# Optimization experiments

Measured on AMD Instinct MI355X. Metric: run time of the kernel, lower is better.

Reference implementation:

```python
import jax, jax.numpy as jnp
import numpy as np

# libmolgrid GridMaker defaults (gnina): resolution 0.5 A, dimension 23.5 A
RES = 0.5
DIM = 23.5
G = int(round(DIM / RES)) + 1  # 48 grid points per axis
N_ATOMS = 800
N_TYPES = 28  # gnina default atom typing


def setup_inputs() -> dict:
    key = jax.random.key(0)
    k1, k2, k3 = jax.random.split(key, 3)
    # atoms spread around the grid center (grid spans +-11.75 A)
    coords = jax.random.normal(k1, (N_ATOMS, 3), dtype=jnp.float32) * 4.0
    # continuous (soft) type vectors in [0,1)
    types = jax.random.uniform(k2, (N_ATOMS, N_TYPES), dtype=jnp.float32)
    # van-der-Waals-like radii in [1.0, 1.8) A
    radii = 1.0 + 0.8 * jax.random.uniform(k3, (N_ATOMS,), dtype=jnp.float32)
    center = jnp.zeros((3,), dtype=jnp.float32)
    return {"center": center, "coords": coords, "types": types, "radii": radii}


def _density(coords, radii, center):
    """Per-atom libmolgrid density on the [G,G,G] grid -> [N,G,G,G].

    f(d) = exp(-2 d^2/r^2)                         for d <  r
         = e^-2 (4 (d/r)^2 - 12 (d/r) + 9)          for r <= d < 1.5 r
         = 0                                        otherwise
    (C1-continuous quadratic tail, libmolgrid defaults grm=1.0, final=1.5).
    """
    origin = center - DIM / 2.0  # [3]
    ax = jnp.arange(G, dtype=jnp.float32) * RES  # [G]
    dx = (origin[0] + ax)[None, :] - coords[:, 0:1]  # [N,G]
    dy = (origin[1] + ax)[None, :] - coords[:, 1:2]
    dz = (origin[2] + ax)[None, :] - coords[:, 2:3]
    d2 = (dx[:, :, None, None] ** 2
          + dy[:, None, :, None] ** 2
          + dz[:, None, None, :] ** 2)  # [N,G,G,G]
    r = radii[:, None, None, None]
    dr2 = d2 / (r * r)
    dr = jnp.sqrt(jnp.maximum(dr2, 1e-12))
    gauss = jnp.exp(-2.0 * dr2)
    inv_e2 = jnp.float32(np.exp(-2.0))
    quad = inv_e2 * (4.0 * dr2 - 12.0 * dr + 9.0)
    return jnp.where(dr < 1.0, gauss, jnp.where(dr < 1.5, quad, 0.0))


def reference(center, coords, types, radii):
    dens = _density(coords, radii, center)  # [N,G,G,G]
    # weight each atom's footprint by its type vector and scatter-sum over atoms
    return jnp.einsum('nxyz,nt->txyz', dens, types)  # [T,G,G,G]
```

## Files before the change

kernel.cpp:

```cpp
#include <hip/hip_runtime.h>

#define GR    48
#define GR2   (GR * GR)
#define GR3   (GR * GR * GR)
#define NA    800
#define NT    28
#define RESF  0.5f
#define HALF_DIM 11.75f
#define INV_E2 0.13533528323661270f

#define TXC   2
#define TYC   2
#define TZC   16
#define NTX   (GR / TXC)
#define NTY   (GR / TYC)
#define NTZ   (GR / TZC)
#define NBLK  (NTX * NTY * NTZ)
#define KB    64
#define KPAD  80

typedef __attribute__((ext_vector_type(8))) short short8;
typedef __attribute__((ext_vector_type(4))) float floatx4;

__device__ inline unsigned short f2bf(float x) {
    unsigned u = __builtin_bit_cast(unsigned, x);
    u = (u + 0x7FFFu + ((u >> 16) & 1u)) >> 16;
    return (unsigned short)u;
}

__global__ __launch_bounds__(256) void c2g_kernel(
    const float* __restrict__ center,
    const float* __restrict__ coords,
    const float* __restrict__ types,
    const float* __restrict__ radii,
    float* __restrict__ out)
{
    __shared__ float4 s_atom[NA];
    __shared__ int    s_ai[NA];
    __shared__ int    s_cnt;
    __shared__ unsigned short s_val[64 * KPAD];
    __shared__ unsigned short s_tT[32 * KPAD];
    __shared__ float  s_out[64 * 33];

    const int tid  = threadIdx.x;
    const int lane = tid & 63;
    const int w    = tid >> 6;
    const int b    = blockIdx.x;
    const int tz   = b % NTZ;
    const int ty   = (b / NTZ) % NTY;
    const int tx   = b / (NTZ * NTY);

    const float ox = center[0] - HALF_DIM;
    const float oy = center[1] - HALF_DIM;
    const float oz = center[2] - HALF_DIM;

    const float bxlo = ox + tx * (TXC * RESF), bxhi = bxlo + (TXC - 1) * RESF;
    const float bylo = oy + ty * (TYC * RESF), byhi = bylo + (TYC - 1) * RESF;
    const float bzlo = oz + tz * (TZC * RESF), bzhi = bzlo + (TZC - 1) * RESF;

    if (tid == 0) s_cnt = 0;
    __syncthreads();

    for (int a0 = 0; a0 < NA; a0 += 256) {
        int a = a0 + tid;
        bool accept = false;
        float ax = 0.f, ay = 0.f, az = 0.f, r = 1.f;
        if (a < NA) {
            ax = coords[3 * a + 0];
            ay = coords[3 * a + 1];
            az = coords[3 * a + 2];
            r  = radii[a];
            float cut = 1.5f * r;
            float ddx = ax - fminf(fmaxf(ax, bxlo), bxhi);
            float ddy = ay - fminf(fmaxf(ay, bylo), byhi);
            float ddz = az - fminf(fmaxf(az, bzlo), bzhi);
            float d2 = fmaf(ddx, ddx, fmaf(ddy, ddy, ddz * ddz));
            accept = d2 < cut * cut;
        }
        unsigned long long m = __ballot(accept);
        if (m) {
            int base = 0;
            if (lane == 0) base = atomicAdd(&s_cnt, __popcll(m));
            base = __shfl(base, 0);
            if (accept) {
                int p = base + __popcll(m & ((1ull << lane) - 1ull));
                s_atom[p] = make_float4(ax, ay, az, 1.0f / (r * r));
                s_ai[p] = a;
            }
        }
    }
    __syncthreads();
    const int cnt = s_cnt;

    const int lzz = lane & 15;
    const int ly2 = (lane >> 4) & 1;
    const int lx2 = lane >> 5;
    const float gx = bxlo + lx2 * RESF;
    const float gy = bylo + ly2 * RESF;
    const float gz = bzlo + lzz * RESF;

    const int lm = lane & 15;
    const int lg = lane >> 4;

    floatx4 acc0 = {0.f, 0.f, 0.f, 0.f};
    floatx4 acc1 = {0.f, 0.f, 0.f, 0.f};

    const int r0 = tid >> 3,         q0 = tid & 7;
    const int r1 = (tid + 256) >> 3, q1 = tid & 7;

    for (int k0 = 0; k0 < cnt; k0 += KB) {
        const int kmax = (cnt - k0 < KB) ? (cnt - k0) : KB;

        float4 tv0 = make_float4(0.f, 0.f, 0.f, 0.f);
        float4 tv1 = tv0;
        if (q0 < 7 && r0 < kmax)
            tv0 = *(const float4*)(types + s_ai[k0 + r0] * NT + q0 * 4);
        if (q1 < 7 && r1 < kmax)
            tv1 = *(const float4*)(types + s_ai[k0 + r1] * NT + q1 * 4);

        unsigned pk[8];
        #pragma unroll
        for (int jj = 0; jj < 8; ++jj) {
            float v[2];
            #pragma unroll
            for (int h = 0; h < 2; ++h) {
                int row = w * 16 + 2 * jj + h;
                float vv = 0.0f;
                if (row < kmax) {
                    float4 at = s_atom[k0 + row];
                    float dx = gx - at.x;
                    float dy = gy - at.y;
                    float dz = gz - at.z;
                    float d2 = fmaf(dx, dx, fmaf(dy, dy, dz * dz));
                    float dr2 = d2 * at.w;
                    float g  = __expf(-2.0f * dr2);
                    float dr = sqrtf(dr2);
                    float q  = INV_E2 * fmaf(4.0f, dr2, fmaf(-12.0f, dr, 9.0f));
                    vv = (dr2 < 1.0f) ? g : ((dr2 < 2.25f) ? q : 0.0f);
                }
                v[h] = vv;
            }
            pk[jj] = (unsigned)f2bf(v[0]) | ((unsigned)f2bf(v[1]) << 16);
        }
        *(uint4*)&s_val[lane * KPAD + w * 16]     = *(uint4*)&pk[0];
        *(uint4*)&s_val[lane * KPAD + w * 16 + 8] = *(uint4*)&pk[4];

        {
            const float* e0 = &tv0.x;
            const float* e1 = &tv1.x;
            #pragma unroll
            for (int i = 0; i < 4; ++i) {
                s_tT[(q0 * 4 + i) * KPAD + r0] = f2bf(e0[i]);
                s_tT[(q1 * 4 + i) * KPAD + r1] = f2bf(e1[i]);
            }
        }
        __syncthreads();

        #pragma unroll
        for (int ks = 0; ks < 2; ++ks) {
            int ko = ks * 32 + lg * 8;
            short8 afr = *(const short8*)&s_val[(w * 16 + lm) * KPAD + ko];
            short8 b0  = *(const short8*)&s_tT[lm * KPAD + ko];
            short8 b1  = *(const short8*)&s_tT[(16 + lm) * KPAD + ko];
            acc0 = __builtin_amdgcn_mfma_f32_16x16x32_bf16(afr, b0, acc0, 0, 0, 0);
            acc1 = __builtin_amdgcn_mfma_f32_16x16x32_bf16(afr, b1, acc1, 0, 0, 0);
        }
        __syncthreads();
    }

    #pragma unroll
    for (int r = 0; r < 4; ++r) {
        int cellO = w * 16 + lg * 4 + r;
        s_out[cellO * 33 + lm]      = acc0[r];
        s_out[cellO * 33 + 16 + lm] = acc1[r];
    }
    __syncthreads();

    #pragma unroll
    for (int i = 0; i < 7; ++i) {
        int idx = i * 256 + tid;
        int t = idx >> 6;
        int c = idx & 63;
        int z = c & 15, y = (c >> 4) & 1, x = c >> 5;
        int gidx = (tx * TXC + x) * GR2 + (ty * TYC + y) * GR + tz * TZC + z;
        out[t * GR3 + gidx] = s_out[c * 33 + t];
    }
}

extern "C" void kernel_launch(void* const* d_in, const int* in_sizes, int n_in,
                              void* d_out, int out_size, void* d_ws, size_t ws_size,
                              hipStream_t stream) {
    const float* center = (const float*)d_in[0];
    const float* coords = (const float*)d_in[1];
    const float* types  = (const float*)d_in[2];
    const float* radii  = (const float*)d_in[3];
    float* out = (float*)d_out;

    c2g_kernel<<<dim3(NBLK), dim3(256), 0, stream>>>(center, coords, types, radii, out);
}
```

Before: 72.06 us.

## Compute density fragments directly in registers and double-buffer type tiles

Swaps the MFMA operand roles so each lane computes its density values straight into the B-fragment registers, which removes the s_val shared-memory staging and one barrier per chunk. Type rows are prefetched from global memory one chunk ahead into a double-buffered LDS tile. The atom list is padded to a multiple of 64 with far-away dummy atoms so the per-row bounds checks go away. Shared memory is also aliased to shrink the footprint, at the cost of extra padding work and a reworked output transpose.

New measurement: 74.72 us. +3.7%, slower.

```diff
diff --git a/kernel.cpp b/kernel.cpp
--- a/kernel.cpp
+++ b/kernel.cpp
@@ -4,6 +4,7 @@
 #define GR2   (GR * GR)
 #define GR3   (GR * GR * GR)
 #define NA    800
+#define NAP   864
 #define NT    28
 #define RESF  0.5f
 #define HALF_DIM 11.75f
@@ -18,6 +19,7 @@
 #define NBLK  (NTX * NTY * NTZ)
 #define KB    64
 #define KPAD  80
+#define TBUF  (32 * KPAD)
 
 typedef __attribute__((ext_vector_type(8))) short short8;
 typedef __attribute__((ext_vector_type(4))) float floatx4;
@@ -35,12 +37,12 @@
     const float* __restrict__ radii,
     float* __restrict__ out)
 {
-    __shared__ float4 s_atom[NA];
-    __shared__ int    s_ai[NA];
-    __shared__ int    s_cnt;
-    __shared__ unsigned short s_val[64 * KPAD];
-    __shared__ unsigned short s_tT[32 * KPAD];
-    __shared__ float  s_out[64 * 33];
+    __shared__ __align__(16) unsigned char smem[NAP * 16 + NAP * 4 + 2 * TBUF * 2];
+    float4*         s_atom = (float4*)smem;
+    int*            s_ai   = (int*)(smem + NAP * 16);
+    unsigned short* s_tT   = (unsigned short*)(smem + NAP * 20);
+    float*          s_out  = (float*)smem;
+    __shared__ int s_cnt;
 
     const int tid  = threadIdx.x;
     const int lane = tid & 63;
@@ -90,89 +92,101 @@
         }
     }
     __syncthreads();
-    const int cnt = s_cnt;
-
-    const int lzz = lane & 15;
-    const int ly2 = (lane >> 4) & 1;
-    const int lx2 = lane >> 5;
-    const float gx = bxlo + lx2 * RESF;
-    const float gy = bylo + ly2 * RESF;
-    const float gz = bzlo + lzz * RESF;
+    const int cnt  = s_cnt;
+    const int cntp = (cnt + 63) & ~63;
+    const int nb   = cntp >> 6;
+
+    for (int i = cnt + tid; i < cntp; i += 256) {
+        s_atom[i] = make_float4(1e9f, 1e9f, 1e9f, 1.0f);
+        s_ai[i] = 0;
+    }
+    __syncthreads();
 
     const int lm = lane & 15;
     const int lg = lane >> 4;
+    const float gx = bxlo + (w >> 1) * RESF;
+    const float gy = bylo + (w & 1) * RESF;
+    const float gz = bzlo + lm * RESF;
+
+    const int r0 = tid >> 3, q0 = tid & 7;
+    const int r1 = r0 + 32;
+
+    auto evalv = [&](int idx) -> float {
+        float4 at = s_atom[idx];
+        float dx = gx - at.x, dy = gy - at.y, dz = gz - at.z;
+        float d2 = fmaf(dx, dx, fmaf(dy, dy, dz * dz));
+        float dr2 = d2 * at.w;
+        float g  = __expf(-2.0f * dr2);
+        float dr = sqrtf(dr2);
+        float qd = INV_E2 * fmaf(4.0f, dr2, fmaf(-12.0f, dr, 9.0f));
+        return (dr2 < 1.0f) ? g : ((dr2 < 2.25f) ? qd : 0.0f);
+    };
+    auto pk2 = [&](int idx) -> unsigned {
+        float a = evalv(idx), bsc = evalv(idx + 1);
+        return (unsigned)f2bf(a) | ((unsigned)f2bf(bsc) << 16);
+    };
+    auto stage = [&](unsigned short* tb, float4 tv, int rr, int qq) {
+        tb[(qq * 4 + 0) * KPAD + rr] = f2bf(tv.x);
+        tb[(qq * 4 + 1) * KPAD + rr] = f2bf(tv.y);
+        tb[(qq * 4 + 2) * KPAD + rr] = f2bf(tv.z);
+        tb[(qq * 4 + 3) * KPAD + rr] = f2bf(tv.w);
+    };
 
     floatx4 acc0 = {0.f, 0.f, 0.f, 0.f};
     floatx4 acc1 = {0.f, 0.f, 0.f, 0.f};
 
-    const int r0 = tid >> 3,         q0 = tid & 7;
-    const int r1 = (tid + 256) >> 3, q1 = tid & 7;
-
-    for (int k0 = 0; k0 < cnt; k0 += KB) {
-        const int kmax = (cnt - k0 < KB) ? (cnt - k0) : KB;
-
-        float4 tv0 = make_float4(0.f, 0.f, 0.f, 0.f);
-        float4 tv1 = tv0;
-        if (q0 < 7 && r0 < kmax)
-            tv0 = *(const float4*)(types + s_ai[k0 + r0] * NT + q0 * 4);
-        if (q1 < 7 && r1 < kmax)
-            tv1 = *(const float4*)(types + s_ai[k0 + r1] * NT + q1 * 4);
-
-        unsigned pk[8];
-        #pragma unroll
-        for (int jj = 0; jj < 8; ++jj) {
-            float v[2];
-            #pragma unroll
-            for (int h = 0; h < 2; ++h) {
-                int row = w * 16 + 2 * jj + h;
-                float vv = 0.0f;
-                if (row < kmax) {
-                    float4 at = s_atom[k0 + row];
-                    float dx = gx - at.x;
-                    float dy = gy - at.y;
-                    float dz = gz - at.z;
-                    float d2 = fmaf(dx, dx, fmaf(dy, dy, dz * dz));
-                    float dr2 = d2 * at.w;
-                    float g  = __expf(-2.0f * dr2);
-                    float dr = sqrtf(dr2);
-                    float q  = INV_E2 * fmaf(4.0f, dr2, fmaf(-12.0f, dr, 9.0f));
-                    vv = (dr2 < 1.0f) ? g : ((dr2 < 2.25f) ? q : 0.0f);
-                }
-                v[h] = vv;
-            }
-            pk[jj] = (unsigned)f2bf(v[0]) | ((unsigned)f2bf(v[1]) << 16);
-        }
-        *(uint4*)&s_val[lane * KPAD + w * 16]     = *(uint4*)&pk[0];
-        *(uint4*)&s_val[lane * KPAD + w * 16 + 8] = *(uint4*)&pk[4];
-
-        {
-            const float* e0 = &tv0.x;
-            const float* e1 = &tv1.x;
-            #pragma unroll
-            for (int i = 0; i < 4; ++i) {
-                s_tT[(q0 * 4 + i) * KPAD + r0] = f2bf(e0[i]);
-                s_tT[(q1 * 4 + i) * KPAD + r1] = f2bf(e1[i]);
-            }
-        }
-        __syncthreads();
-
-        #pragma unroll
-        for (int ks = 0; ks < 2; ++ks) {
-            int ko = ks * 32 + lg * 8;
-            short8 afr = *(const short8*)&s_val[(w * 16 + lm) * KPAD + ko];
-            short8 b0  = *(const short8*)&s_tT[lm * KPAD + ko];
-            short8 b1  = *(const short8*)&s_tT[(16 + lm) * KPAD + ko];
-            acc0 = __builtin_amdgcn_mfma_f32_16x16x32_bf16(afr, b0, acc0, 0, 0, 0);
-            acc1 = __builtin_amdgcn_mfma_f32_16x16x32_bf16(afr, b1, acc1, 0, 0, 0);
+    if (nb > 0) {
+        float4 t0 = make_float4(0.f, 0.f, 0.f, 0.f), t1 = t0;
+        if (q0 < 7) {
+            t0 = *(const float4*)(types + s_ai[r0] * NT + q0 * 4);
+            t1 = *(const float4*)(types + s_ai[r1] * NT + q0 * 4);
+        }
+        stage(s_tT, t0, r0, q0);
+        stage(s_tT, t1, r1, q0);
+    }
+    __syncthreads();
+
+    for (int bi = 0; bi < nb; ++bi) {
+        const int k0  = bi * KB;
+        const int cur = bi & 1;
+        const unsigned short* tb = s_tT + cur * TBUF;
+        unsigned short* tbn = s_tT + (cur ^ 1) * TBUF;
+
+        float4 t0 = make_float4(0.f, 0.f, 0.f, 0.f), t1 = t0;
+        const bool have_next = (bi + 1 < nb);
+        if (have_next && q0 < 7) {
+            t0 = *(const float4*)(types + s_ai[k0 + KB + r0] * NT + q0 * 4);
+            t1 = *(const float4*)(types + s_ai[k0 + KB + r1] * NT + q0 * 4);
+        }
+
+        const int base0 = k0 + lg * 8;
+        const int base1 = k0 + 32 + lg * 8;
+        short8 bf0 = __builtin_bit_cast(short8,
+            make_uint4(pk2(base0), pk2(base0 + 2), pk2(base0 + 4), pk2(base0 + 6)));
+        short8 bf1 = __builtin_bit_cast(short8,
+            make_uint4(pk2(base1), pk2(base1 + 2), pk2(base1 + 4), pk2(base1 + 6)));
+
+        short8 a00 = *(const short8*)&tb[lm * KPAD + lg * 8];
+        short8 a10 = *(const short8*)&tb[(16 + lm) * KPAD + lg * 8];
+        acc0 = __builtin_amdgcn_mfma_f32_16x16x32_bf16(a00, bf0, acc0, 0, 0, 0);
+        acc1 = __builtin_amdgcn_mfma_f32_16x16x32_bf16(a10, bf0, acc1, 0, 0, 0);
+        short8 a01 = *(const short8*)&tb[lm * KPAD + 32 + lg * 8];
+        short8 a11 = *(const short8*)&tb[(16 + lm) * KPAD + 32 + lg * 8];
+        acc0 = __builtin_amdgcn_mfma_f32_16x16x32_bf16(a01, bf1, acc0, 0, 0, 0);
+        acc1 = __builtin_amdgcn_mfma_f32_16x16x32_bf16(a11, bf1, acc1, 0, 0, 0);
+
+        if (have_next) {
+            stage(tbn, t0, r0, q0);
+            stage(tbn, t1, r1, q0);
         }
         __syncthreads();
     }
 
     #pragma unroll
     for (int r = 0; r < 4; ++r) {
-        int cellO = w * 16 + lg * 4 + r;
-        s_out[cellO * 33 + lm]      = acc0[r];
-        s_out[cellO * 33 + 16 + lm] = acc1[r];
+        int c = w * 16 + lm;
+        s_out[c * 33 + lg * 4 + r]      = acc0[r];
+        s_out[c * 33 + 16 + lg * 4 + r] = acc1[r];
     }
     __syncthreads();
 
```
